# Kernel tuning notes

Hardware: AMD Instinct MI355X
Metric: run time of the kernel (lower is better)

## Reference

```python
import jax, jax.numpy as jnp
import numpy as np

NUM_ACTIONS = 16  # number of unique leaf actions (= output_dim)


def setup_inputs() -> dict:
    key = jax.random.key(0)
    ks = jax.random.split(key, 7)
    B, IN, D, A = 32768, 128, 511, 512
    L = D + A + 1  # 1024 leaves
    x = jax.random.normal(ks[0], (B, IN), dtype=jnp.float32)
    Wd = jax.random.normal(ks[1], (D, IN), dtype=jnp.float32) * 0.05
    bd = jax.random.normal(ks[2], (D,), dtype=jnp.float32) * 0.05
    Wa = jax.random.normal(ks[3], (A, IN), dtype=jnp.float32) * 0.05
    ba = jax.random.normal(ks[4], (A,), dtype=jnp.float32) * 0.05
    Wl = jax.random.normal(ks[5], (L, 2 * (D + A)), dtype=jnp.float32) * 0.05
    seg_ids = jax.random.randint(ks[6], (L,), 0, NUM_ACTIONS, dtype=jnp.int32)
    return {"x": x, "Wd": Wd, "bd": bd, "Wa": Wa, "ba": ba, "Wl": Wl,
            "seg_ids": seg_ids}


def reference(x, Wd, bd, Wa, ba, Wl, seg_ids):
    # dual linear heads (torch Linear: y = x @ W.T + b)
    x1 = x @ Wd.T + bd            # [B, D]
    x2 = x @ Wa.T + ba            # [B, A]
    h = jnp.concatenate([x1, x2], axis=1)                     # [B, D+A]
    hh = jnp.concatenate([jax.nn.relu(h), jax.nn.relu(-h)], axis=1)  # [B, 2(D+A)]
    leaf = hh @ Wl.T              # [B, L]
    # ragged per-action max over leaf columns (MaxPoolLayer)
    pooled = jax.ops.segment_max(leaf.T, seg_ids,
                                 num_segments=NUM_ACTIONS).T   # [B, NUM_ACTIONS]
    return jax.nn.softmax(pooled, axis=-1)
```

## Files before the change

### kernel.cpp

```cpp
#include <hip/hip_runtime.h>
#include <hip/hip_bf16.h>
#include <cstdint>
#include <cmath>

#define AS1 __attribute__((address_space(1)))
#define AS3 __attribute__((address_space(3)))

typedef unsigned short u16;
typedef uint32_t u32;
typedef __attribute__((ext_vector_type(8))) __bf16 bf16x8;
typedef __attribute__((ext_vector_type(8))) unsigned short u16x8;
typedef __attribute__((ext_vector_type(4))) float f32x4;

__device__ __forceinline__ u16 f2bf(float f) {
    uint32_t u = __builtin_bit_cast(uint32_t, f);
    return (u16)((u + 0x7fffu + ((u >> 16) & 1u)) >> 16);
}

__device__ __forceinline__ u32 f2ord(float f) {
    u32 u = __builtin_bit_cast(u32, f);
    return u ^ (u32)(((int32_t)u >> 31) | 0x80000000);
}
__device__ __forceinline__ float ord2f(u32 v) {
    u32 u = (v & 0x80000000u) ? (v ^ 0x80000000u) : ~v;
    return __builtin_bit_cast(float, u);
}

__global__ void setup_all(const float* __restrict__ x,
                          const float* __restrict__ Wd, const float* __restrict__ bd,
                          const float* __restrict__ Wa, const float* __restrict__ ba,
                          const float* __restrict__ Wl,
                          u16* __restrict__ xb, u16* __restrict__ w1b,
                          float* __restrict__ bb, u16* __restrict__ w1t,
                          u16* __restrict__ wsb, u16* __restrict__ dlb,
                          float* __restrict__ cl) {
    __shared__ float cred[256];
    const int b = blockIdx.x;
    const int tid = threadIdx.x;
    if (b < 2048) {
        long idx = (long)(b * 256 + tid) * 8;
        float4 a = *(const float4*)(x + idx);
        float4 c = *(const float4*)(x + idx + 4);
        u16x8 o;
        o[0]=f2bf(a.x); o[1]=f2bf(a.y); o[2]=f2bf(a.z); o[3]=f2bf(a.w);
        o[4]=f2bf(c.x); o[5]=f2bf(c.y); o[6]=f2bf(c.z); o[7]=f2bf(c.w);
        *(u16x8*)(xb + idx) = o;
    } else if (b < 2112) {
        int t = (b - 2048) * 256 + tid;
        int row = t >> 4, g = (t & 15) * 8;
        const float* src = nullptr;
        if (row < 511)       src = Wd + row * 128 + g;
        else if (row < 1023) src = Wa + (row - 511) * 128 + g;
        u16x8 o = 0;
        if (src) {
            #pragma unroll
            for (int j = 0; j < 8; ++j) o[j] = f2bf(src[j]);
        }
        *(u16x8*)(w1b + row * 128 + g) = o;
        #pragma unroll
        for (int j = 0; j < 8; ++j) w1t[(g + j) * 1024 + row] = o[j];
        if ((t & 15) == 0)
            bb[row] = row < 511 ? bd[row] : (row < 1023 ? ba[row - 511] : 0.f);
    } else {
        const int l0 = (b - 2112) * 2;
        const int lo = tid >> 7, g = (tid & 127) * 8;
        const float* src = Wl + (long)(l0 + lo) * 2046;
        u16x8 os, od;
        float part = 0.f;
        #pragma unroll
        for (int j = 0; j < 8; ++j) {
            int c = g + j;
            float pa = 0.f, pb = 0.f;
            if (c < 1023) { pa = src[c]; pb = src[1023 + c]; }
            os[j] = f2bf(0.5f * (pa + pb));
            float v = pa - pb;
            od[j] = f2bf(v);
            float b1 = c < 511 ? bd[c] : (c < 1023 ? ba[c - 511] : 0.f);
            part += v * b1;
        }
        *(u16x8*)(wsb + (long)(l0 + lo) * 1024 + g) = os;
        *(u16x8*)(dlb + (long)(l0 + lo) * 1024 + g) = od;
        cred[tid] = part;
        __syncthreads();
        if (tid < 2) {
            float s = 0.f;
            #pragma unroll
            for (int k = 0; k < 128; ++k) s += cred[tid * 128 + k];
            cl[l0 + tid] = 0.5f * s;
        }
    }
}

__global__ __launch_bounds__(256) void gemm_hwc(
        const u16* __restrict__ xb, const u16* __restrict__ w1b,
        const float* __restrict__ bb,
        const u16* __restrict__ dlb, const u16* __restrict__ w1t,
        u16* __restrict__ habs, u16* __restrict__ wcb) {
    __shared__ union SharedU {
        struct { u16 As[2][4096]; u16 Bs[2][4096]; } s;
        u16 obuf[128 * 132];
    } sh;
    const int tid  = threadIdx.x;
    const int lane = tid & 63, wave = tid >> 6;
    const int wy = wave >> 1, wx = wave & 1;
    const int i16 = lane & 15, q = lane >> 4;
    const int cA = wave * 2, srow = lane >> 2, scol = (lane & 3) * 8;

    f32x4 acc[4][4];
    #pragma unroll
    for (int m = 0; m < 4; ++m)
        #pragma unroll
        for (int n = 0; n < 4; ++n) acc[m][n] = f32x4{0.f,0.f,0.f,0.f};

    if (blockIdx.y == 0) {
        const long blockM = (long)blockIdx.x * 128;
        const int koff = (blockIdx.x * 4) & 31;
        const u16* a0 = dlb + (blockM + cA * 16 + srow) * 1024 + scol;
        const u16* a1 = dlb + (blockM + (cA + 1) * 16 + srow) * 1024 + scol;
        const u16* b0 = w1t + (long)(cA * 16 + srow) * 1024 + scol;
        const u16* b1 = w1t + (long)((cA + 1) * 16 + srow) * 1024 + scol;
        for (int it = 0; it < 32; ++it) {
            const int k0 = ((it + koff) & 31) << 5;
            __builtin_amdgcn_global_load_lds((const AS1 void*)(a0 + k0), (AS3 void*)&sh.s.As[0][cA * 512],       16, 0, 0);
            __builtin_amdgcn_global_load_lds((const AS1 void*)(a1 + k0), (AS3 void*)&sh.s.As[0][(cA + 1) * 512], 16, 0, 0);
            __builtin_amdgcn_global_load_lds((const AS1 void*)(b0 + k0), (AS3 void*)&sh.s.Bs[0][cA * 512],       16, 0, 0);
            __builtin_amdgcn_global_load_lds((const AS1 void*)(b1 + k0), (AS3 void*)&sh.s.Bs[0][(cA + 1) * 512], 16, 0, 0);
            __syncthreads();
            bf16x8 af[4], bfv[4];
            #pragma unroll
            for (int s = 0; s < 4; ++s) {
                af[s]  = *(const bf16x8*)&sh.s.As[0][(wy * 64 + s * 16 + i16) * 32 + q * 8];
                bfv[s] = *(const bf16x8*)&sh.s.Bs[0][(wx * 64 + s * 16 + i16) * 32 + q * 8];
            }
            #pragma unroll
            for (int sm = 0; sm < 4; ++sm)
                #pragma unroll
                for (int sn = 0; sn < 4; ++sn)
                    acc[sm][sn] = __builtin_amdgcn_mfma_f32_16x16x32_bf16(af[sm], bfv[sn], acc[sm][sn], 0, 0, 0);
            __syncthreads();
        }
        #pragma unroll
        for (int sm = 0; sm < 4; ++sm)
            #pragma unroll
            for (int sn = 0; sn < 4; ++sn) {
                const int col = wx * 64 + sn * 16 + i16;
                #pragma unroll
                for (int r = 0; r < 4; ++r) {
                    const long row = blockM + wy * 64 + sm * 16 + 4 * q + r;
                    wcb[row * 128 + col] = f2bf(0.5f * acc[sm][sn][r]);
                }
            }
        return;
    }

    const int xcd = blockIdx.x, yy = blockIdx.y - 1;
    const long blockM = (long)(xcd * 32 + (yy >> 3)) * 128;
    const int  blockN = (yy & 7) * 128;
    const int  koff = (yy >> 3) & 1;

    const u16* a0 = xb + (blockM + cA * 16 + srow) * 128 + scol;
    const u16* a1 = xb + (blockM + (cA + 1) * 16 + srow) * 128 + scol;
    const u16* b0 = w1b + ((long)blockN + cA * 16 + srow) * 128 + scol;
    const u16* b1 = w1b + ((long)blockN + (cA + 1) * 16 + srow) * 128 + scol;
    for (int it = 0; it < 2; ++it) {
        const int k0 = ((it + koff) & 1) << 6;
        #pragma unroll
        for (int p = 0; p < 2; ++p) {
            const int kp = k0 + p * 32;
            __builtin_amdgcn_global_load_lds((const AS1 void*)(a0 + kp), (AS3 void*)&sh.s.As[p][cA * 512],       16, 0, 0);
            __builtin_amdgcn_global_load_lds((const AS1 void*)(a1 + kp), (AS3 void*)&sh.s.As[p][(cA + 1) * 512], 16, 0, 0);
            __builtin_amdgcn_global_load_lds((const AS1 void*)(b0 + kp), (AS3 void*)&sh.s.Bs[p][cA * 512],       16, 0, 0);
            __builtin_amdgcn_global_load_lds((const AS1 void*)(b1 + kp), (AS3 void*)&sh.s.Bs[p][(cA + 1) * 512], 16, 0, 0);
        }
        __syncthreads();
        #pragma unroll
        for (int p = 0; p < 2; ++p) {
            bf16x8 af[4], bfv[4];
            #pragma unroll
            for (int s = 0; s < 4; ++s) {
                af[s]  = *(const bf16x8*)&sh.s.As[p][(wy * 64 + s * 16 + i16) * 32 + q * 8];
                bfv[s] = *(const bf16x8*)&sh.s.Bs[p][(wx * 64 + s * 16 + i16) * 32 + q * 8];
            }
            #pragma unroll
            for (int sm = 0; sm < 4; ++sm)
                #pragma unroll
                for (int sn = 0; sn < 4; ++sn)
                    acc[sm][sn] = __builtin_amdgcn_mfma_f32_16x16x32_bf16(af[sm], bfv[sn], acc[sm][sn], 0, 0, 0);
        }
        __syncthreads();
    }

    float bv[4];
    #pragma unroll
    for (int sn = 0; sn < 4; ++sn) bv[sn] = bb[blockN + wx * 64 + sn * 16 + i16];
    #pragma unroll
    for (int sm = 0; sm < 4; ++sm)
        #pragma unroll
        for (int sn = 0; sn < 4; ++sn)
            #pragma unroll
            for (int r = 0; r < 4; ++r)
                sh.obuf[(wy * 64 + sm * 16 + 4 * q + r) * 132 + wx * 64 + sn * 16 + i16] =
                    f2bf(fabsf(acc[sm][sn][r] + bv[sn]));
    __syncthreads();
    const int cg = (tid & 15) * 8;
    #pragma unroll
    for (int it = 0; it < 8; ++it) {
        const int row = it * 16 + (tid >> 4);
        *(u16x8*)&habs[(blockM + row) * 1024 + blockN + cg] =
            *(const u16x8*)&sh.obuf[row * 132 + cg];
    }
}

#define NT 18
__global__ __launch_bounds__(512, 2) void gemm_leaf(const u16* __restrict__ habs,
        const u16* __restrict__ xb, const u16* __restrict__ wsb,
        const u16* __restrict__ wcb, const float* __restrict__ cl,
        const int* __restrict__ seg, u32* __restrict__ pp) {
    __shared__ u16 As[2][2][256 * 32];
    __shared__ u16 Bs[2][2][256 * 32];
    __shared__ u32 pmax[256 * 17];

    const int tid  = threadIdx.x;
    const int lane = tid & 63, w = tid >> 6;
    const int wm = w >> 2, wn = w & 3;
    const int i16 = lane & 15, q = lane >> 4;

    const int bid  = blockIdx.x;
    const int wgid = (bid & 7) * 64 + (bid >> 3);
    const int mT = wgid >> 2, nT = wgid & 3;
    const long blockM = (long)mT * 256;
    const int  blockN = nT * 256;

    #pragma unroll
    for (int j = 0; j < 9; ++j) {
        int idx = tid + j * 512;
        if (idx < 256 * 17) pmax[idx] = 0u;
    }

    const int r0 = tid >> 2, c0 = (tid & 3) * 8;
    const u16* gA1 = habs + (blockM + r0) * 1024 + c0;
    const u16* gB1 = wsb  + (long)(blockN + r0) * 1024 + c0;
    const u16* gA2 = xb   + (blockM + r0) * 128 + c0;
    const u16* gB2 = wcb  + (long)(blockN + r0) * 128 + c0;
    const int ldsb = w * 512;

    auto stage = [&](int t, int isB, int kk) {
        u16* dst = (isB ? &Bs[t & 1][kk][0] : &As[t & 1][kk][0]) + ldsb;
        const u16* g;
        int jstr;
        if (t < 16) { g = (isB ? gB1 : gA1) + t * 64 + kk * 32;        jstr = 128 * 1024; }
        else        { g = (isB ? gB2 : gA2) + (t - 16) * 64 + kk * 32; jstr = 128 * 128; }
        __builtin_amdgcn_global_load_lds((const AS1 void*)g,          (AS3 void*)dst,          16, 0, 0);
        __builtin_amdgcn_global_load_lds((const AS1 void*)(g + jstr), (AS3 void*)(dst + 4096), 16, 0, 0);
    };

    f32x4 acc[8][4];
    #pragma unroll
    for (int m = 0; m < 8; ++m)
        #pragma unroll
        for (int n = 0; n < 4; ++n) acc[m][n] = f32x4{0.f,0.f,0.f,0.f};
    bf16x8 areg[8], breg[2];

    auto lda = [&](int slot, int kk) {
        #pragma unroll
        for (int mf = 0; mf < 8; ++mf)
            areg[mf] = *(const bf16x8*)&As[slot][kk][(wm * 128 + mf * 16 + i16) * 32 + q * 8];
    };
    auto ldb = [&](int slot, int kk, int nh) {
        #pragma unroll
        for (int nf = 0; nf < 2; ++nf)
            breg[nf] = *(const bf16x8*)&Bs[slot][kk][(wn * 64 + nh * 32 + nf * 16 + i16) * 32 + q * 8];
    };
    auto mfma16 = [&](int nh) {
        #pragma unroll
        for (int mf = 0; mf < 8; ++mf)
            #pragma unroll
            for (int nf = 0; nf < 2; ++nf)
                acc[mf][nh * 2 + nf] = __builtin_amdgcn_mfma_f32_16x16x32_bf16(
                    areg[mf], breg[nf], acc[mf][nh * 2 + nf], 0, 0, 0);
    };

    stage(0, 0, 0); stage(0, 1, 0); stage(0, 0, 1); stage(0, 1, 1);
    stage(1, 0, 0); stage(1, 1, 0); stage(1, 0, 1);
    asm volatile("s_waitcnt vmcnt(10)" ::: "memory");
    __builtin_amdgcn_s_barrier();

    for (int t = 0; t < NT; ++t) {
        const int slot = t & 1;
        lda(slot, 0); ldb(slot, 0, 0);
        if (t + 1 < NT) stage(t + 1, 1, 1);
        __builtin_amdgcn_s_barrier();
        asm volatile("s_waitcnt lgkmcnt(0)" ::: "memory");
        __builtin_amdgcn_sched_barrier(0);
        __builtin_amdgcn_s_setprio(1);
        mfma16(0);
        __builtin_amdgcn_s_setprio(0);
        __builtin_amdgcn_s_barrier();
        ldb(slot, 0, 1);
        if (t + 2 < NT) stage(t + 2, 0, 0);
        __builtin_amdgcn_s_barrier();
        asm volatile("s_waitcnt lgkmcnt(0)" ::: "memory");
        __builtin_amdgcn_sched_barrier(0);
        __builtin_amdgcn_s_setprio(1);
        mfma16(1);
        __builtin_amdgcn_s_setprio(0);
        if (t < 16)      { asm volatile("s_waitcnt vmcnt(10)" ::: "memory"); }
        else if (t == 16){ asm volatile("s_waitcnt vmcnt(8)"  ::: "memory"); }
        else             { asm volatile("s_waitcnt vmcnt(0)"  ::: "memory"); }
        __builtin_amdgcn_s_barrier();
        lda(slot, 1); ldb(slot, 1, 0);
        if (t + 2 < NT) stage(t + 2, 1, 0);
        __builtin_amdgcn_s_barrier();
        asm volatile("s_waitcnt lgkmcnt(0)" ::: "memory");
        __builtin_amdgcn_sched_barrier(0);
        __builtin_amdgcn_s_setprio(1);
        mfma16(0);
        __builtin_amdgcn_s_setprio(0);
        __builtin_amdgcn_s_barrier();
        ldb(slot, 1, 1);
        if (t + 2 < NT) stage(t + 2, 0, 1);
        __builtin_amdgcn_s_barrier();
        asm volatile("s_waitcnt lgkmcnt(0)" ::: "memory");
        __builtin_amdgcn_sched_barrier(0);
        __builtin_amdgcn_s_setprio(1);
        mfma16(1);
        __builtin_amdgcn_s_setprio(0);
        if (t < 16)      { asm volatile("s_waitcnt vmcnt(10)" ::: "memory"); }
        else if (t == 16){ asm volatile("s_waitcnt vmcnt(4)"  ::: "memory"); }
        __builtin_amdgcn_s_barrier();
    }

    int segc[4]; float clv[4];
    #pragma unroll
    for (int nf = 0; nf < 4; ++nf) {
        const int col = blockN + wn * 64 + nf * 16 + i16;
        segc[nf] = seg[col];
        clv[nf]  = cl[col];
    }
    #pragma unroll
    for (int mf = 0; mf < 8; ++mf)
        #pragma unroll
        for (int nf = 0; nf < 4; ++nf)
            #pragma unroll
            for (int r = 0; r < 4; ++r) {
                const int rl = wm * 128 + mf * 16 + 4 * q + r;
                atomicMax(&pmax[rl * 17 + segc[nf]], f2ord(acc[mf][nf][r] + clv[nf]));
            }
    __syncthreads();
    #pragma unroll
    for (int j = 0; j < 8; ++j) {
        int idx = tid + j * 512;
        pp[((long)nT << 19) + ((blockM + (idx >> 4)) << 4) + (idx & 15)] =
            pmax[(idx >> 4) * 17 + (idx & 15)];
    }
}

__global__ __launch_bounds__(256) void finalize(const u32* __restrict__ pp,
                                                float* __restrict__ out) {
    const int tid = threadIdx.x;
    const long row = (long)blockIdx.x * 16 + (tid >> 4);
    const int t = tid & 15;
    u32 m = 0;
    #pragma unroll
    for (int p = 0; p < 4; ++p)
        m = max(m, pp[((long)p << 19) + (row << 4) + t]);
    float logit = ord2f(m);
    float rm = logit;
    #pragma unroll
    for (int d = 8; d >= 1; d >>= 1) rm = fmaxf(rm, __shfl_xor(rm, d, 16));
    float e = __expf(logit - rm);
    float s = e;
    #pragma unroll
    for (int d = 8; d >= 1; d >>= 1) s += __shfl_xor(s, d, 16);
    out[(row << 4) + t] = e / s;
}

extern "C" void kernel_launch(void* const* d_in, const int* in_sizes, int n_in,
                              void* d_out, int out_size, void* d_ws, size_t ws_size,
                              hipStream_t stream) {
    const float* x  = (const float*)d_in[0];
    const float* Wd = (const float*)d_in[1];
    const float* bd = (const float*)d_in[2];
    const float* Wa = (const float*)d_in[3];
    const float* ba = (const float*)d_in[4];
    const float* Wl = (const float*)d_in[5];
    const int*  seg = (const int*)d_in[6];
    float* out = (float*)d_out;

    char* ws = (char*)d_ws;
    u16*   xb   = (u16*)(ws);
    u16*   w1b  = (u16*)(ws + 8388608);
    float* bb   = (float*)(ws + 8650752);
    u16*   w1t  = (u16*)(ws + 8654848);
    u16*   wsb  = (u16*)(ws + 8916992);
    u16*   dlb  = (u16*)(ws + 11014144);
    u16*   wcb  = (u16*)(ws + 13111296);
    float* clp  = (float*)(ws + 13373440);
    u16*   habs = (u16*)(ws + 13377536);
    u32*   pp   = (u32*)(ws + 80486400);

    setup_all<<<2624, 256, 0, stream>>>(x, Wd, bd, Wa, ba, Wl,
                                        xb, w1b, bb, w1t, wsb, dlb, clp);
    gemm_hwc <<<dim3(8, 257), 256, 0, stream>>>(xb, w1b, bb, dlb, w1t, habs, wcb);
    gemm_leaf<<<dim3(512), 512, 0, stream>>>(habs, xb, wsb, wcb, clp, seg, pp);
    finalize <<<2048, 256, 0, stream>>>(pp, out);
}
```

Before: 225.5 us.

## Swizzle LDS tiles and restructure leaf GEMM into 4-slot K=32 pipeline

Applies an XOR swizzle to the LDS column layout in both GEMM kernels, meant to remove bank conflicts on the bf16x8 fragment reads. The leaf GEMM's K loop is rebuilt from 18 double-buffered 64-wide steps into 36 steps of width 32 over four LDS slots, staging A and B two steps ahead and splitting the MFMA work by M halves instead of N halves. The padded pmax stride (17 to 16) is also dropped, which may bring back bank conflicts in the atomicMax epilogue. The new wait counts and prefetch depth shift the load/compute overlap and add more barriers per unit of K.

```diff
diff --git a/kernel.cpp b/kernel.cpp
--- a/kernel.cpp
+++ b/kernel.cpp
@@ -25,6 +25,7 @@
     u32 u = (v & 0x80000000u) ? (v ^ 0x80000000u) : ~v;
     return __builtin_bit_cast(float, u);
 }
+
 
 __global__ void setup_all(const float* __restrict__ x,
                           const float* __restrict__ Wd, const float* __restrict__ bd,
@@ -104,7 +105,9 @@
     const int lane = tid & 63, wave = tid >> 6;
     const int wy = wave >> 1, wx = wave & 1;
     const int i16 = lane & 15, q = lane >> 4;
-    const int cA = wave * 2, srow = lane >> 2, scol = (lane & 3) * 8;
+    const int cA = wave * 2, srow = lane >> 2;
+    const int scol = (((lane & 3) ^ ((lane >> 3) & 3))) * 8;
+    const int qa   = (q ^ ((i16 >> 1) & 3)) * 8;
 
     f32x4 acc[4][4];
     #pragma unroll
@@ -129,8 +132,8 @@
             bf16x8 af[4], bfv[4];
             #pragma unroll
             for (int s = 0; s < 4; ++s) {
-                af[s]  = *(const bf16x8*)&sh.s.As[0][(wy * 64 + s * 16 + i16) * 32 + q * 8];
-                bfv[s] = *(const bf16x8*)&sh.s.Bs[0][(wx * 64 + s * 16 + i16) * 32 + q * 8];
+                af[s]  = *(const bf16x8*)&sh.s.As[0][(wy * 64 + s * 16 + i16) * 32 + qa];
+                bfv[s] = *(const bf16x8*)&sh.s.Bs[0][(wx * 64 + s * 16 + i16) * 32 + qa];
             }
             #pragma unroll
             for (int sm = 0; sm < 4; ++sm)
@@ -178,8 +181,8 @@
             bf16x8 af[4], bfv[4];
             #pragma unroll
             for (int s = 0; s < 4; ++s) {
-                af[s]  = *(const bf16x8*)&sh.s.As[p][(wy * 64 + s * 16 + i16) * 32 + q * 8];
-                bfv[s] = *(const bf16x8*)&sh.s.Bs[p][(wx * 64 + s * 16 + i16) * 32 + q * 8];
+                af[s]  = *(const bf16x8*)&sh.s.As[p][(wy * 64 + s * 16 + i16) * 32 + qa];
+                bfv[s] = *(const bf16x8*)&sh.s.Bs[p][(wx * 64 + s * 16 + i16) * 32 + qa];
             }
             #pragma unroll
             for (int sm = 0; sm < 4; ++sm)
@@ -211,15 +214,13 @@
     }
 }
 
-#define NT 18
 __global__ __launch_bounds__(512, 2) void gemm_leaf(const u16* __restrict__ habs,
         const u16* __restrict__ xb, const u16* __restrict__ wsb,
         const u16* __restrict__ wcb, const float* __restrict__ cl,
         const int* __restrict__ seg, u32* __restrict__ pp) {
-    __shared__ u16 As[2][2][256 * 32];
-    __shared__ u16 Bs[2][2][256 * 32];
-    __shared__ u32 pmax[256 * 17];
-
+    __shared__ __align__(16) u16 As[4][256 * 32];
+    __shared__ __align__(16) u16 Bs[4][256 * 32];
+    __shared__ u32 pmax[256 * 16];
     const int tid  = threadIdx.x;
     const int lane = tid & 63, w = tid >> 6;
     const int wm = w >> 2, wn = w & 3;
@@ -232,101 +233,85 @@
     const int  blockN = nT * 256;
 
     #pragma unroll
-    for (int j = 0; j < 9; ++j) {
-        int idx = tid + j * 512;
-        if (idx < 256 * 17) pmax[idx] = 0u;
-    }
-
-    const int r0 = tid >> 2, c0 = (tid & 3) * 8;
-    const u16* gA1 = habs + (blockM + r0) * 1024 + c0;
-    const u16* gB1 = wsb  + (long)(blockN + r0) * 1024 + c0;
-    const u16* gA2 = xb   + (blockM + r0) * 128 + c0;
-    const u16* gB2 = wcb  + (long)(blockN + r0) * 128 + c0;
+    for (int j = 0; j < 8; ++j) pmax[tid + j * 512] = 0u;
+
+    const int r0 = tid >> 2;
+    const int scol = (((tid & 3) ^ ((tid >> 3) & 3))) * 8;
+    const u16* gA1 = habs + (blockM + r0) * 1024 + scol;
+    const u16* gB1 = wsb  + (long)(blockN + r0) * 1024 + scol;
+    const u16* gA2 = xb   + (blockM + r0) * 128 + scol;
+    const u16* gB2 = wcb  + (long)(blockN + r0) * 128 + scol;
     const int ldsb = w * 512;
 
-    auto stage = [&](int t, int isB, int kk) {
-        u16* dst = (isB ? &Bs[t & 1][kk][0] : &As[t & 1][kk][0]) + ldsb;
-        const u16* g;
-        int jstr;
-        if (t < 16) { g = (isB ? gB1 : gA1) + t * 64 + kk * 32;        jstr = 128 * 1024; }
-        else        { g = (isB ? gB2 : gA2) + (t - 16) * 64 + kk * 32; jstr = 128 * 128; }
+    auto stageA = [&](int tt) {
+        u16* dst = &As[tt & 3][ldsb];
+        const u16* g; int jstr;
+        if (tt < 32) { g = gA1 + tt * 32;        jstr = 128 * 1024; }
+        else         { g = gA2 + (tt - 32) * 32; jstr = 128 * 128; }
         __builtin_amdgcn_global_load_lds((const AS1 void*)g,          (AS3 void*)dst,          16, 0, 0);
         __builtin_amdgcn_global_load_lds((const AS1 void*)(g + jstr), (AS3 void*)(dst + 4096), 16, 0, 0);
     };
+    auto stageB = [&](int tt) {
+        u16* dst = &Bs[tt & 3][ldsb];
+        const u16* g; int jstr;
+        if (tt < 32) { g = gB1 + tt * 32;        jstr = 128 * 1024; }
+        else         { g = gB2 + (tt - 32) * 32; jstr = 128 * 128; }
+        __builtin_amdgcn_global_load_lds((const AS1 void*)g,          (AS3 void*)dst,          16, 0, 0);
+        __builtin_amdgcn_global_load_lds((const AS1 void*)(g + jstr), (AS3 void*)(dst + 4096), 16, 0, 0);
+    };
 
     f32x4 acc[8][4];
     #pragma unroll
     for (int m = 0; m < 8; ++m)
         #pragma unroll
         for (int n = 0; n < 4; ++n) acc[m][n] = f32x4{0.f,0.f,0.f,0.f};
-    bf16x8 areg[8], breg[2];
-
-    auto lda = [&](int slot, int kk) {
-        #pragma unroll
-        for (int mf = 0; mf < 8; ++mf)
-            areg[mf] = *(const bf16x8*)&As[slot][kk][(wm * 128 + mf * 16 + i16) * 32 + q * 8];
-    };
-    auto ldb = [&](int slot, int kk, int nh) {
-        #pragma unroll
-        for (int nf = 0; nf < 2; ++nf)
-            breg[nf] = *(const bf16x8*)&Bs[slot][kk][(wn * 64 + nh * 32 + nf * 16 + i16) * 32 + q * 8];
-    };
-    auto mfma16 = [&](int nh) {
-        #pragma unroll
-        for (int mf = 0; mf < 8; ++mf)
-            #pragma unroll
-            for (int nf = 0; nf < 2; ++nf)
-                acc[mf][nh * 2 + nf] = __builtin_amdgcn_mfma_f32_16x16x32_bf16(
-                    areg[mf], breg[nf], acc[mf][nh * 2 + nf], 0, 0, 0);
-    };
-
-    stage(0, 0, 0); stage(0, 1, 0); stage(0, 0, 1); stage(0, 1, 1);
-    stage(1, 0, 0); stage(1, 1, 0); stage(1, 0, 1);
-    asm volatile("s_waitcnt vmcnt(10)" ::: "memory");
+    bf16x8 areg[4], breg[4];
+
+    const int rdc = (q ^ ((i16 >> 1) & 3)) * 8;
+    auto lda = [&](int slot, int mh) {
+        #pragma unroll
+        for (int mf = 0; mf < 4; ++mf)
+            areg[mf] = *(const bf16x8*)&As[slot][(wm * 128 + mh * 64 + mf * 16 + i16) * 32 + rdc];
+    };
+    auto ldb = [&](int slot) {
+        #pragma unroll
+        for (int nf = 0; nf < 4; ++nf)
+            breg[nf] = *(const bf16x8*)&Bs[slot][(wn * 64 + nf * 16 + i16) * 32 + rdc];
+    };
+    auto mf16 = [&](int mh) {
+        #pragma unroll
+        for (int mf = 0; mf < 4; ++mf)
+            #pragma unroll
+            for (int nf = 0; nf < 4; ++nf)
+                acc[mh * 4 + mf][nf] = __builtin_amdgcn_mfma_f32_16x16x32_bf16(
+                    areg[mf], breg[nf], acc[mh * 4 + mf][nf], 0, 0, 0);
+    };
+
+    stageA(0); stageB(0); stageA(1); stageB(1);
+    asm volatile("s_waitcnt vmcnt(4)" ::: "memory");
     __builtin_amdgcn_s_barrier();
 
-    for (int t = 0; t < NT; ++t) {
-        const int slot = t & 1;
-        lda(slot, 0); ldb(slot, 0, 0);
-        if (t + 1 < NT) stage(t + 1, 1, 1);
+    for (int t = 0; t < 36; ++t) {
+        const int slot = t & 3;
+        lda(slot, 0); ldb(slot);
+        if (t + 2 < 36) stageA(t + 2);
         __builtin_amdgcn_s_barrier();
         asm volatile("s_waitcnt lgkmcnt(0)" ::: "memory");
         __builtin_amdgcn_sched_barrier(0);
         __builtin_amdgcn_s_setprio(1);
-        mfma16(0);
+        mf16(0);
         __builtin_amdgcn_s_setprio(0);
         __builtin_amdgcn_s_barrier();
-        ldb(slot, 0, 1);
-        if (t + 2 < NT) stage(t + 2, 0, 0);
+        lda(slot, 1);
+        if (t + 2 < 36) stageB(t + 2);
         __builtin_amdgcn_s_barrier();
         asm volatile("s_waitcnt lgkmcnt(0)" ::: "memory");
         __builtin_amdgcn_sched_barrier(0);
         __builtin_amdgcn_s_setprio(1);
-        mfma16(1);
+        mf16(1);
         __builtin_amdgcn_s_setprio(0);
-        if (t < 16)      { asm volatile("s_waitcnt vmcnt(10)" ::: "memory"); }
-        else if (t == 16){ asm volatile("s_waitcnt vmcnt(8)"  ::: "memory"); }
-        else             { asm volatile("s_waitcnt vmcnt(0)"  ::: "memory"); }
-        __builtin_amdgcn_s_barrier();
-        lda(slot, 1); ldb(slot, 1, 0);
-        if (t + 2 < NT) stage(t + 2, 1, 0);
-        __builtin_amdgcn_s_barrier();
-        asm volatile("s_waitcnt lgkmcnt(0)" ::: "memory");
-        __builtin_amdgcn_sched_barrier(0);
-        __builtin_amdgcn_s_setprio(1);
-        mfma16(0);
-        __builtin_amdgcn_s_setprio(0);
-        __builtin_amdgcn_s_barrier();
-        ldb(slot, 1, 1);
-        if (t + 2 < NT) stage(t + 2, 0, 1);
-        __builtin_amdgcn_s_barrier();
-        asm volatile("s_waitcnt lgkmcnt(0)" ::: "memory");
-        __builtin_amdgcn_sched_barrier(0);
-        __builtin_amdgcn_s_setprio(1);
-        mfma16(1);
-        __builtin_amdgcn_s_setprio(0);
-        if (t < 16)      { asm volatile("s_waitcnt vmcnt(10)" ::: "memory"); }
-        else if (t == 16){ asm volatile("s_waitcnt vmcnt(4)"  ::: "memory"); }
+        if (t < 34)       { asm volatile("s_waitcnt vmcnt(4)" ::: "memory"); }
+        else if (t == 34) { asm volatile("s_waitcnt vmcnt(0)" ::: "memory"); }
         __builtin_amdgcn_s_barrier();
     }
 
@@ -344,14 +329,13 @@
             #pragma unroll
             for (int r = 0; r < 4; ++r) {
                 const int rl = wm * 128 + mf * 16 + 4 * q + r;
-                atomicMax(&pmax[rl * 17 + segc[nf]], f2ord(acc[mf][nf][r] + clv[nf]));
+                atomicMax(&pmax[rl * 16 + segc[nf]], f2ord(acc[mf][nf][r] + clv[nf]));
             }
     __syncthreads();
     #pragma unroll
     for (int j = 0; j < 8; ++j) {
         int idx = tid + j * 512;
-        pp[((long)nT << 19) + ((blockM + (idx >> 4)) << 4) + (idx & 15)] =
-            pmax[(idx >> 4) * 17 + (idx & 15)];
+        pp[((long)nT << 19) + ((blockM + (idx >> 4)) << 4) + (idx & 15)] = pmax[idx];
     }
 }
 
```

Result: faster. 207.1 us (-8.2%).
